# Kernel tuning notes

Hardware: AMD Instinct MI355X
Metric: run time of the kernel (lower is better)

The kernel has to match this reference:

```python
import jax, jax.numpy as jnp
import numpy as np

N = 100000        # nodes
E = 3200000       # edges per support (avg degree 32)
D_IN, D_OUT = 256, 128
ATT_H = 32
ALPHA, BETA = 0.5, 0.5  # FLAGS.alpha / FLAGS.beta


def setup_inputs() -> dict:
    key = jax.random.key(0)
    ks = jax.random.split(key, 10)
    x = jax.random.normal(ks[0], (N, D_IN), dtype=jnp.float32)
    glorot = lambda k, shp: jax.random.uniform(k, shp, jnp.float32,
                                               -np.sqrt(6.0 / sum(shp)), np.sqrt(6.0 / sum(shp)))
    Wa = glorot(ks[1], (D_IN, D_OUT))
    Wb = glorot(ks[2], (D_IN, D_OUT))
    Wc = glorot(ks[3], (D_IN, D_OUT))
    attn_w1 = glorot(ks[4], (D_OUT, ATT_H))
    attn_b1 = jnp.zeros((ATT_H,), jnp.float32)
    attn_w2 = glorot(ks[5], (ATT_H, 1))
    rows = jax.random.randint(ks[6], (7, E), 0, N, dtype=jnp.int32)
    cols = jax.random.randint(ks[7], (7, E), 0, N, dtype=jnp.int32)
    # normalized-adjacency-like positive values, scaled ~1/degree
    vals = jax.random.uniform(ks[8], (7, E), jnp.float32) * (1.0 / 32.0)
    return {"x": x, "Wa": Wa, "Wb": Wb, "Wc": Wc,
            "attn_w1": attn_w1, "attn_b1": attn_b1, "attn_w2": attn_w2,
            "rows": rows, "cols": cols, "vals": vals}


def reference(x, Wa, Wb, Wc, attn_w1, attn_b1, attn_w2, rows, cols, vals):
    n = x.shape[0]

    def spmm(i, X):
        # support[i] @ X via COO gather-scale-scatter: memory-bound SpMM
        return jax.ops.segment_sum(vals[i][:, None] * X[cols[i]], rows[i], num_segments=n)

    def bilinear_pooling(i, X):
        s = spmm(i, X)
        return 0.5 * (s * s - spmm(i, X * X))

    pre_a = x @ Wa                    # [N, D_OUT]
    pre_b = x @ Wb
    _ = x @ Wc                        # computed in original, never used
    sec_ord = 0.5 * (pre_a * pre_a - pre_a * pre_b)
    pre_al = pre_a + sec_ord

    emb = jnp.stack([pre_a, pre_al], axis=1)          # [N, 2, D_OUT]
    h = jnp.tanh(emb @ attn_w1 + attn_b1)             # [N, 2, 32]
    att = jax.nn.softmax(h @ attn_w2, axis=1)         # [N, 2, 1]
    pre_sup = jnp.sum(att * emb, axis=1)              # [N, D_OUT]

    out_gcn = spmm(0, pre_sup)
    out_bi1 = spmm(5, bilinear_pooling(1, pre_sup) - bilinear_pooling(3, pre_sup))
    out_bi2 = spmm(6, bilinear_pooling(2, pre_sup) - bilinear_pooling(4, pre_sup))
    out_bi = (1.0 - BETA) * out_bi1 + BETA * out_bi2
    output = (1.0 - ALPHA) * out_gcn + ALPHA * out_bi
    return jax.nn.relu(output)
```

## Files before the change

### kernel.cpp

```cpp
#include <hip/hip_runtime.h>

typedef unsigned int uint;
typedef unsigned short ushort;

__device__ __forceinline__ float bfl(uint u){ return __uint_as_float(u << 16); }
__device__ __forceinline__ float bfh(uint u){ return __uint_as_float(u & 0xFFFF0000u); }
__device__ __forceinline__ uint f2bfbits(float f){
    uint b = __float_as_uint(f);
    return (b + 0x7FFFu + ((b >> 16) & 1u)) >> 16;
}
__device__ __forceinline__ uint packbf2(float a, float b){
    return f2bfbits(a) | (f2bfbits(b) << 16);
}
__device__ __forceinline__ int smap(int4 m, int s){
    return (s == 0) ? m.x : (s == 1) ? m.y : (s == 2) ? m.z : m.w;
}
__device__ __forceinline__ int2 ldnt(const int2* p){
    long long v = __builtin_nontemporal_load((const long long*)p);
    int2 r; r.x = (int)(v & 0xFFFFFFFFll); r.y = (int)(v >> 32); return r;
}

#define CH 6144
#define SBSHIFT 7
#define SBROWS 128
#define HISTP 784
#define SBUF_CAP 5120
#define CACHE_PT 20
#define PGRID 2048


#define BM 64
#define BK 32
__global__ __launch_bounds__(256) void gemm_kernel(const float* __restrict__ x,
                                                   const float* __restrict__ Wa,
                                                   const float* __restrict__ Wb,
                                                   float* __restrict__ AB, int N) {
    __shared__ float xsT[BK][BM + 4];
    __shared__ float wsm[BK][256];
    int t = threadIdx.x;
    int rowbase = blockIdx.x * BM;
    int tx = t & 15, ty = t >> 4;
    float acc[4][16];
    #pragma unroll
    for (int i = 0; i < 4; i++)
        #pragma unroll
        for (int j = 0; j < 16; j++) acc[i][j] = 0.f;

    for (int k0 = 0; k0 < 256; k0 += BK) {
        {
            int r = t & 63;
            int koff = (t >> 6) * 8;
            int gr = rowbase + r; if (gr >= N) gr = N - 1;
            const float* src = x + (size_t)gr * 256 + k0 + koff;
            float4 u0 = *(const float4*)(src);
            float4 u1 = *(const float4*)(src + 4);
            xsT[koff + 0][r] = u0.x; xsT[koff + 1][r] = u0.y;
            xsT[koff + 2][r] = u0.z; xsT[koff + 3][r] = u0.w;
            xsT[koff + 4][r] = u1.x; xsT[koff + 5][r] = u1.y;
            xsT[koff + 6][r] = u1.z; xsT[koff + 7][r] = u1.w;
        }
        {
            #pragma unroll
            for (int i = 0; i < 8; i++) {
                int f = t + i * 256;
                int rr = f >> 6, c4 = f & 63;
                const float* src = (c4 < 32) ? &Wa[(size_t)(k0 + rr) * 128 + c4 * 4]
                                             : &Wb[(size_t)(k0 + rr) * 128 + (c4 - 32) * 4];
                *(float4*)&wsm[rr][c4 * 4] = *(const float4*)src;
            }
        }
        __syncthreads();
        #pragma unroll
        for (int kk = 0; kk < BK; ++kk) {
            float4 a = *(const float4*)&xsT[kk][ty * 4];
            float av[4] = {a.x, a.y, a.z, a.w};
            float bv[16];
            #pragma unroll
            for (int q = 0; q < 4; q++)
                *(float4*)&bv[q * 4] = *(const float4*)&wsm[kk][q * 64 + tx * 4];
            #pragma unroll
            for (int i = 0; i < 4; i++)
                #pragma unroll
                for (int j = 0; j < 16; j++)
                    acc[i][j] = fmaf(av[i], bv[j], acc[i][j]);
        }
        __syncthreads();
    }
    #pragma unroll
    for (int i = 0; i < 4; i++) {
        int gr = rowbase + ty * 4 + i;
        if (gr < N) {
            #pragma unroll
            for (int q = 0; q < 4; q++) {
                float4 o = {acc[i][q*4], acc[i][q*4+1], acc[i][q*4+2], acc[i][q*4+3]};
                *(float4*)&AB[(size_t)gr * 256 + q * 64 + tx * 4] = o;
            }
        }
    }
}

__global__ __launch_bounds__(256) void attn_kernel(const float* __restrict__ AB,
        const float* __restrict__ w1, const float* __restrict__ b1,
        const float* __restrict__ w2, uint* __restrict__ Pb, int N) {
    __shared__ float w1s[128 * 32];
    __shared__ float b1s[32], w2s[32];
    __shared__ float aS[4][128], alS[4][128];
    int t = threadIdx.x;
    #pragma unroll
    for (int i = 0; i < 16; i++) w1s[t + i * 256] = w1[t + i * 256];
    if (t < 32) { b1s[t] = b1[t]; w2s[t] = w2[t]; }

    int w = t >> 6, lane = t & 63;
    int node = blockIdx.x * 4 + w;
    bool active = node < N;
    int nclamp = active ? node : (N - 1);
    float2 a = *(const float2*)(AB + (size_t)nclamp * 256 + lane * 2);
    float2 b = *(const float2*)(AB + (size_t)nclamp * 256 + 128 + lane * 2);
    float2 al;
    al.x = a.x + 0.5f * (a.x * a.x - a.x * b.x);
    al.y = a.y + 0.5f * (a.y * a.y - a.y * b.y);
    aS[w][lane * 2] = a.x;   aS[w][lane * 2 + 1] = a.y;
    alS[w][lane * 2] = al.x; alS[w][lane * 2 + 1] = al.y;
    __syncthreads();

    int j = lane & 31;
    const float* src = (lane < 32) ? aS[w] : alS[w];
    float acc = b1s[j];
    #pragma unroll 8
    for (int d = 0; d < 128; ++d) acc = fmaf(src[d], w1s[d * 32 + j], acc);
    float h = tanhf(acc);
    float prod = h * w2s[j];
    #pragma unroll
    for (int off = 1; off < 32; off <<= 1) prod += __shfl_xor(prod, off);
    float eo = __shfl_xor(prod, 32);
    float e0 = (lane < 32) ? prod : eo;
    float e1 = (lane < 32) ? eo : prod;
    float m = fmaxf(e0, e1);
    float p0 = expf(e0 - m), p1 = expf(e1 - m);
    float inv = 1.0f / (p0 + p1);
    float at0 = p0 * inv, at1 = p1 * inv;
    if (active) {
        float px = at0 * a.x + at1 * al.x;
        float py = at0 * a.y + at1 * al.y;
        Pb[(size_t)node * 64 + lane] = packbf2(px, py);
    }
}


__device__ __forceinline__ void block_scan1024(int* a, int t, int* wsum) {
    int lane = t & 63, wid = t >> 6;
    int c0 = a[t * 4], c1 = a[t * 4 + 1], c2 = a[t * 4 + 2], c3 = a[t * 4 + 3];
    int tsum = c0 + c1 + c2 + c3, incl = tsum;
    #pragma unroll
    for (int off = 1; off < 64; off <<= 1) {
        int y = __shfl_up(incl, off);
        if (lane >= off) incl += y;
    }
    if (lane == 63) wsum[wid] = incl;
    __syncthreads();
    int wb = 0;
    #pragma unroll
    for (int w = 0; w < 4; w++) if (w < wid) wb += wsum[w];
    int excl = wb + incl - tsum;
    a[t * 4] = excl; a[t * 4 + 1] = excl + c0;
    a[t * 4 + 2] = excl + c0 + c1; a[t * 4 + 3] = excl + c0 + c1 + c2;
    __syncthreads();
}

__global__ __launch_bounds__(256) void count_chunk(const int* __restrict__ rows, int4 map,
        int* __restrict__ lenTab, int* __restrict__ gtot, int NSB, int nchunks, int E) {
    __shared__ int hist[HISTP];
    int c = blockIdx.x, s = blockIdx.y, t = threadIdx.x;
    size_t sb = (size_t)smap(map, s) * E;
    int e0 = c * CH, e1 = e0 + CH; if (e1 > E) e1 = E;
    for (int i = t; i < HISTP; i += 256) hist[i] = 0;
    __syncthreads();
    for (int e = e0 + t; e < e1; e += 256)
        atomicAdd(&hist[(uint)rows[sb + e] >> SBSHIFT], 1);
    __syncthreads();
    for (int b = t; b < NSB; b += 256) {
        int l = hist[b];
        lenTab[((size_t)s * NSB + b) * nchunks + c] = l;
        if (l) atomicAdd(&gtot[s * NSB + b], l);
    }
}

__global__ __launch_bounds__(256) void bucket_scanex(const int* __restrict__ gtot,
        int* __restrict__ bbase, int NSB) {
    __shared__ int a[1024];
    __shared__ int wsum[4];
    int s = blockIdx.x, t = threadIdx.x;
    #pragma unroll
    for (int k = 0; k < 4; k++) {
        int i = t + k * 256;
        a[i] = (i < NSB) ? gtot[s * NSB + i] : 0;
    }
    __syncthreads();
    block_scan1024(a, t, wsum);
    #pragma unroll
    for (int k = 0; k < 4; k++) {
        int i = t + k * 256;
        if (i <= NSB) bbase[s * (NSB + 1) + i] = a[i];
    }
}

__global__ __launch_bounds__(64) void pos_scan(const int* __restrict__ lenTab,
        const int* __restrict__ bbase, int* __restrict__ segPos, int NSB, int nchunks) {
    int b = blockIdx.x, s = blockIdx.y, lane = threadIdx.x;
    const int* lt = lenTab + ((size_t)s * NSB + b) * nchunks;
    int* sp = segPos + ((size_t)s * NSB + b) * nchunks;
    int run = bbase[s * (NSB + 1) + b];
    for (int c0 = 0; c0 < nchunks; c0 += 64) {
        int c = c0 + lane;
        int v = (c < nchunks) ? lt[c] : 0;
        int incl = v;
        #pragma unroll
        for (int off = 1; off < 64; off <<= 1) {
            int y = __shfl_up(incl, off);
            if (lane >= off) incl += y;
        }
        if (c < nchunks) sp[c] = run + incl - v;
        run += __shfl(incl, 63);
    }
}

__global__ __launch_bounds__(256) void place_chunk(const int* __restrict__ rows,
        const int* __restrict__ cols, const float* __restrict__ vals, int4 map,
        const int* __restrict__ segPos, int2* __restrict__ stage2,
        int NSB, int nchunks, int E) {
    __shared__ int2 sbuf[CH];
    __shared__ ushort bmap[CH];
    __shared__ int cur[1024];
    __shared__ int off[1024];
    __shared__ int spos[HISTP];
    __shared__ int wsum[4];
    int c = blockIdx.x, s = blockIdx.y, t = threadIdx.x;
    size_t sb = (size_t)smap(map, s) * E;
    int e0 = c * CH, e1 = e0 + CH; if (e1 > E) e1 = E;
    int csz = e1 - e0;
    #pragma unroll
    for (int k = 0; k < 4; k++) cur[t + k * 256] = 0;
    __syncthreads();
    for (int e = e0 + t; e < e1; e += 256)
        atomicAdd(&cur[(uint)rows[sb + e] >> SBSHIFT], 1);
    __syncthreads();
    block_scan1024(cur, t, wsum);
    #pragma unroll
    for (int k = 0; k < 4; k++) { int i = t + k * 256; off[i] = cur[i]; }
    for (int b = t; b < NSB; b += 256)
        spos[b] = segPos[((size_t)s * NSB + b) * nchunks + c];
    __syncthreads();
    for (int e = e0 + t; e < e1; e += 256) {
        int r = rows[sb + e];
        int b = (uint)r >> SBSHIFT;
        int pos = atomicAdd(&cur[b], 1);
        uint cw = (uint)cols[sb + e] | ((uint)(r & (SBROWS - 1)) << 20);
        sbuf[pos] = make_int2((int)cw, __float_as_int(vals[sb + e]));
        bmap[pos] = (ushort)b;
    }
    __syncthreads();
    int2* dst = stage2 + (size_t)s * E;
    for (int i = t; i < csz; i += 256) {
        int b = bmap[i];
        dst[spos[b] + (i - off[b])] = sbuf[i];
    }
}

__global__ __launch_bounds__(256) void fill_bucket(const int2* __restrict__ stage2,
        const int* __restrict__ bbase, int* __restrict__ rp, int2* __restrict__ pk,
        int NSB, int N, int E) {
    __shared__ int2 sbuf[SBUF_CAP];
    __shared__ int cur[128];
    __shared__ int loc[132];
    __shared__ int wsum2[2];
    int b = blockIdx.x, s = blockIdx.y, t = threadIdx.x;
    int lane = t & 63, wid = t >> 6;
    int rowbase = b << SBSHIFT;
    int nrows = N - rowbase; if (nrows > SBROWS) nrows = SBROWS;
    size_t sb = (size_t)s * E;
    int beg = bbase[s * (NSB + 1) + b];
    int end = bbase[s * (NSB + 1) + b + 1];
    int tot = end - beg;
    if (t < 128) cur[t] = 0;
    __syncthreads();
    int2 myE[CACHE_PT];
    #pragma unroll
    for (int k = 0; k < CACHE_PT; k++) {
        int idx = t + k * 256;
        if (idx < tot) {
            int2 u = stage2[sb + beg + idx];
            myE[k] = u;
            atomicAdd(&cur[((uint)u.x) >> 20], 1);
        }
    }
    for (int idx = t + CACHE_PT * 256; idx < tot; idx += 256) {
        int2 u = stage2[sb + beg + idx];
        atomicAdd(&cur[((uint)u.x) >> 20], 1);
    }
    __syncthreads();
    int v = 0, incl = 0;
    if (t < 128) {
        v = cur[t]; incl = v;
        #pragma unroll
        for (int off = 1; off < 64; off <<= 1) {
            int y = __shfl_up(incl, off);
            if (lane >= off) incl += y;
        }
        if (lane == 63) wsum2[wid] = incl;
    }
    __syncthreads();
    if (t < 128) {
        int excl = incl - v + ((wid == 1) ? wsum2[0] : 0);
        loc[t] = excl; cur[t] = excl;
        if (t < nrows) rp[(size_t)s * (N + 1) + rowbase + t] = beg + excl;
    }
    if (t == 0) loc[128] = tot;
    if (b == 0 && t == 0) rp[(size_t)s * (N + 1) + N] = E;
    __syncthreads();
    #pragma unroll
    for (int k = 0; k < CACHE_PT; k++) {
        int idx = t + k * 256;
        if (idx < tot) {
            int2 u = myE[k];
            int lr = ((uint)u.x) >> 20;
            int pos = atomicAdd(&cur[lr], 1);
            int2 w = make_int2(u.x & 0xFFFFF, u.y);
            if (pos < SBUF_CAP) sbuf[pos] = w; else pk[sb + beg + pos] = w;
        }
    }
    for (int idx = t + CACHE_PT * 256; idx < tot; idx += 256) {
        int2 u = stage2[sb + beg + idx];
        int lr = ((uint)u.x) >> 20;
        int pos = atomicAdd(&cur[lr], 1);
        int2 w = make_int2(u.x & 0xFFFFF, u.y);
        if (pos < SBUF_CAP) sbuf[pos] = w; else pk[sb + beg + pos] = w;
    }
    __syncthreads();
    for (int r = wid; r < nrows; r += 4) {
        int rb = loc[r], re = loc[r + 1];
        int deg = re - rb;
        if (deg < 2 || deg > 64 || re > SBUF_CAP) continue;
        int key = 0x7FFFFFFF, val = 0;
        if (lane < deg) { int2 u = sbuf[rb + lane]; key = u.x; val = u.y; }
        #pragma unroll
        for (int k = 2; k <= 64; k <<= 1) {
            #pragma unroll
            for (int j = k >> 1; j > 0; j >>= 1) {
                int okey = __shfl_xor(key, j);
                int oval = __shfl_xor(val, j);
                bool up = ((lane & k) == 0);
                bool lower = ((lane & j) == 0);
                bool keepmin = (lower == up);
                bool take = keepmin ? (okey < key) : (okey > key);
                if (take) { key = okey; val = oval; }
            }
        }
        if (lane < deg) sbuf[rb + lane] = make_int2(key, val);
    }
    __syncthreads();
    int lim = (tot < SBUF_CAP) ? tot : SBUF_CAP;
    for (int i = t; i < lim; i += 256)
        __builtin_nontemporal_store(*(const long long*)&sbuf[i], (long long*)&pk[sb + beg + i]);
}


__device__ __forceinline__ void row_gather_sum(const int2* __restrict__ pk,
        int e, int end, const uint* __restrict__ Xb, int lane,
        float& ax, float& ay) {
    for (; e + 4 <= end; e += 4) {
        int2 c0 = ldnt(&pk[e]);     int2 c1 = ldnt(&pk[e + 1]);
        int2 c2 = ldnt(&pk[e + 2]); int2 c3 = ldnt(&pk[e + 3]);
        uint u0 = Xb[(c0.x << 6) + lane]; uint u1 = Xb[(c1.x << 6) + lane];
        uint u2 = Xb[(c2.x << 6) + lane]; uint u3 = Xb[(c3.x << 6) + lane];
        float v0 = __int_as_float(c0.y), v1 = __int_as_float(c1.y);
        float v2 = __int_as_float(c2.y), v3 = __int_as_float(c3.y);
        ax = fmaf(v0, bfl(u0), ax); ay = fmaf(v0, bfh(u0), ay);
        ax = fmaf(v1, bfl(u1), ax); ay = fmaf(v1, bfh(u1), ay);
        ax = fmaf(v2, bfl(u2), ax); ay = fmaf(v2, bfh(u2), ay);
        ax = fmaf(v3, bfl(u3), ax); ay = fmaf(v3, bfh(u3), ay);
    }
    for (; e < end; ++e) {
        int2 c0 = ldnt(&pk[e]);
        uint u0 = Xb[(c0.x << 6) + lane];
        float v0 = __int_as_float(c0.y);
        ax = fmaf(v0, bfl(u0), ax); ay = fmaf(v0, bfh(u0), ay);
    }
}

__device__ __forceinline__ void row_gather_bp(const int2* __restrict__ pk,
        int e, int end, const uint* __restrict__ Xb, int lane,
        float& sx, float& sy, float& qx, float& qy) {
    for (; e + 4 <= end; e += 4) {
        int2 c0 = ldnt(&pk[e]);     int2 c1 = ldnt(&pk[e + 1]);
        int2 c2 = ldnt(&pk[e + 2]); int2 c3 = ldnt(&pk[e + 3]);
        uint u0 = Xb[(c0.x << 6) + lane]; uint u1 = Xb[(c1.x << 6) + lane];
        uint u2 = Xb[(c2.x << 6) + lane]; uint u3 = Xb[(c3.x << 6) + lane];
        float v0 = __int_as_float(c0.y), v1 = __int_as_float(c1.y);
        float v2 = __int_as_float(c2.y), v3 = __int_as_float(c3.y);
        float x0 = bfl(u0), y0 = bfh(u0), x1 = bfl(u1), y1 = bfh(u1);
        float x2 = bfl(u2), y2 = bfh(u2), x3 = bfl(u3), y3 = bfh(u3);
        sx = fmaf(v0, x0, sx); sy = fmaf(v0, y0, sy);
        qx = fmaf(v0 * x0, x0, qx); qy = fmaf(v0 * y0, y0, qy);
        sx = fmaf(v1, x1, sx); sy = fmaf(v1, y1, sy);
        qx = fmaf(v1 * x1, x1, qx); qy = fmaf(v1 * y1, y1, qy);
        sx = fmaf(v2, x2, sx); sy = fmaf(v2, y2, sy);
        qx = fmaf(v2 * x2, x2, qx); qy = fmaf(v2 * y2, y2, qy);
        sx = fmaf(v3, x3, sx); sy = fmaf(v3, y3, sy);
        qx = fmaf(v3 * x3, x3, qx); qy = fmaf(v3 * y3, y3, qy);
    }
    for (; e < end; ++e) {
        int2 c0 = ldnt(&pk[e]);
        uint u0 = Xb[(c0.x << 6) + lane];
        float v0 = __int_as_float(c0.y);
        float x0 = bfl(u0), y0 = bfh(u0);
        sx = fmaf(v0, x0, sx); sy = fmaf(v0, y0, sy);
        qx = fmaf(v0 * x0, x0, qx); qy = fmaf(v0 * y0, y0, qy);
    }
}

__global__ __launch_bounds__(256) void spmm_bp2(const int* __restrict__ rpA,
        const int2* __restrict__ pkA, const int* __restrict__ rpB,
        const int2* __restrict__ pkB, const uint* __restrict__ Xb,
        uint* __restrict__ outb, int N) {
    int w = threadIdx.x >> 6, lane = threadIdx.x & 63;
    int stride = gridDim.x * 4;
    for (int row = blockIdx.x * 4 + w; row < N; row += stride) {
        float sax = 0.f, say = 0.f, qax = 0.f, qay = 0.f;
        float sbx = 0.f, sby = 0.f, qbx = 0.f, qby = 0.f;
        row_gather_bp(pkA, rpA[row], rpA[row + 1], Xb, lane, sax, say, qax, qay);
        row_gather_bp(pkB, rpB[row], rpB[row + 1], Xb, lane, sbx, sby, qbx, qby);
        float tx = 0.5f * ((sax * sax - qax) - (sbx * sbx - qbx));
        float ty = 0.5f * ((say * say - qay) - (sby * sby - qby));
        outb[((size_t)row << 6) + lane] = packbf2(tx, ty);
    }
}

__global__ __launch_bounds__(256) void spmm_out(const int* __restrict__ rp0,
        const int2* __restrict__ pk0, const int* __restrict__ rp5,
        const int2* __restrict__ pk5, const int* __restrict__ rp6,
        const int2* __restrict__ pk6, const uint* __restrict__ Pb,
        const uint* __restrict__ t1b, const uint* __restrict__ t2b,
        float* __restrict__ out, int N) {
    int w = threadIdx.x >> 6, lane = threadIdx.x & 63;
    int stride = gridDim.x * 4;
    for (int row = blockIdx.x * 4 + w; row < N; row += stride) {
        float a0x = 0.f, a0y = 0.f, a5x = 0.f, a5y = 0.f, a6x = 0.f, a6y = 0.f;
        row_gather_sum(pk0, rp0[row], rp0[row + 1], Pb,  lane, a0x, a0y);
        row_gather_sum(pk5, rp5[row], rp5[row + 1], t1b, lane, a5x, a5y);
        row_gather_sum(pk6, rp6[row], rp6[row + 1], t2b, lane, a6x, a6y);
        float rx = fmaxf(0.5f * a0x + 0.25f * a5x + 0.25f * a6x, 0.f);
        float ry = fmaxf(0.5f * a0y + 0.25f * a5y + 0.25f * a6y, 0.f);
        *(float2*)(out + ((size_t)row << 7) + (lane << 1)) = make_float2(rx, ry);
    }
}


extern "C" void kernel_launch(void* const* d_in, const int* in_sizes, int n_in,
                              void* d_out, int out_size, void* d_ws, size_t ws_size,
                              hipStream_t stream) {
    (void)n_in; (void)out_size; (void)ws_size;
    const float* x   = (const float*)d_in[0];
    const float* Wa  = (const float*)d_in[1];
    const float* Wb  = (const float*)d_in[2];
    const float* w1  = (const float*)d_in[4];
    const float* b1  = (const float*)d_in[5];
    const float* w2  = (const float*)d_in[6];
    const int* rows  = (const int*)d_in[7];
    const int* cols  = (const int*)d_in[8];
    const float* vals = (const float*)d_in[9];
    float* out = (float*)d_out;

    const int N = in_sizes[0] / 256;
    const int E = in_sizes[7] / 7;
    const int NSB = (N + SBROWS - 1) >> SBSHIFT;
    const int nchunks = (E + CH - 1) / CH;

    uint* Pb  = (uint*)d_ws;
    uint* t1b = Pb + (size_t)N * 64;
    uint* t2b = t1b + (size_t)N * 64;
    int2* pk  = (int2*)(t2b + (size_t)N * 64);
    size_t regionFloats = (size_t)N * 256;
    if ((size_t)8 * E > regionFloats) regionFloats = (size_t)8 * E;
    int2* stage2 = pk + (size_t)4 * E;
    float* AB    = (float*)stage2;
    int* rp      = (int*)((float*)stage2 + regionFloats);
    int* lenTab  = rp + 4 * (size_t)(N + 1);
    int* segPos  = lenTab + (size_t)4 * NSB * nchunks;
    int* gtot    = segPos + (size_t)4 * NSB * nchunks;
    int* bbase   = gtot + (size_t)4 * NSB;

    dim3 b256(256);
    int sgrid = (N + 3) / 4;
    int pgrid = PGRID; if (pgrid > sgrid) pgrid = sgrid;

    gemm_kernel<<<(N + BM - 1) / BM, b256, 0, stream>>>(x, Wa, Wb, AB, N);
    attn_kernel<<<sgrid, b256, 0, stream>>>(AB, w1, b1, w2, Pb, N);

    auto build = [&](int4 map, int nsup) {
        hipMemsetAsync(gtot, 0, (size_t)nsup * NSB * sizeof(int), stream);
        count_chunk<<<dim3(nchunks, nsup), b256, 0, stream>>>(rows, map, lenTab, gtot,
                                                              NSB, nchunks, E);
        bucket_scanex<<<nsup, b256, 0, stream>>>(gtot, bbase, NSB);
        pos_scan<<<dim3(NSB, nsup), dim3(64), 0, stream>>>(lenTab, bbase, segPos, NSB, nchunks);
        place_chunk<<<dim3(nchunks, nsup), b256, 0, stream>>>(rows, cols, vals, map,
                                                              segPos, stage2, NSB, nchunks, E);
        fill_bucket<<<dim3(NSB, nsup), b256, 0, stream>>>(stage2, bbase, rp, pk, NSB, N, E);
    };

    const int NP1 = N + 1;

    build(make_int4(1, 3, 2, 4), 4);
    spmm_bp2<<<pgrid, b256, 0, stream>>>(rp + 0 * NP1, pk + 0 * (size_t)E,
                                         rp + 1 * NP1, pk + 1 * (size_t)E, Pb, t1b, N);
    spmm_bp2<<<pgrid, b256, 0, stream>>>(rp + 2 * NP1, pk + 2 * (size_t)E,
                                         rp + 3 * NP1, pk + 3 * (size_t)E, Pb, t2b, N);

    build(make_int4(0, 5, 6, 6), 3);
    spmm_out<<<pgrid, b256, 0, stream>>>(rp + 0 * NP1, pk + 0 * (size_t)E,
                                         rp + 1 * NP1, pk + 1 * (size_t)E,
                                         rp + 2 * NP1, pk + 2 * (size_t)E,
                                         Pb, t1b, t2b, out, N);
}
```

Baseline: 2.195 ms.

## Batch CSR build of all seven supports and drop global bucket atomics

When the workspace is large enough, the bucketed CSR build runs for all seven supports in a single batched set of kernels instead of two passes of four and three. Global bucket totals now come from a separate reduction over the per-chunk length table, replacing the memset and per-bucket atomics. Chunk block indices are also swizzled across XCDs. The batching uses more workspace and falls back to the old two-pass path otherwise.

```diff
diff --git a/kernel.cpp b/kernel.cpp
--- a/kernel.cpp
+++ b/kernel.cpp
@@ -12,12 +12,19 @@
 __device__ __forceinline__ uint packbf2(float a, float b){
     return f2bfbits(a) | (f2bfbits(b) << 16);
 }
-__device__ __forceinline__ int smap(int4 m, int s){
-    return (s == 0) ? m.x : (s == 1) ? m.y : (s == 2) ? m.z : m.w;
+__device__ __forceinline__ int smap8(int4 lo, int4 hi, int s){
+    int4 m = (s < 4) ? lo : hi;
+    int k = s & 3;
+    return (k == 0) ? m.x : (k == 1) ? m.y : (k == 2) ? m.z : m.w;
 }
 __device__ __forceinline__ int2 ldnt(const int2* p){
     long long v = __builtin_nontemporal_load((const long long*)p);
     int2 r; r.x = (int)(v & 0xFFFFFFFFll); r.y = (int)(v >> 32); return r;
+}
+__device__ __forceinline__ int xcd_swz(int bid, int n){
+    int q = n >> 3, r = n & 7;
+    int x = bid & 7, i = bid >> 3;
+    return (x < r) ? (x * (q + 1) + i) : (r * (q + 1) + (x - r) * q + i);
 }
 
 #define CH 6144
@@ -167,25 +174,35 @@
     __syncthreads();
 }
 
-__global__ __launch_bounds__(256) void count_chunk(const int* __restrict__ rows, int4 map,
-        int* __restrict__ lenTab, int* __restrict__ gtot, int NSB, int nchunks, int E) {
+__global__ __launch_bounds__(256) void count_chunk(const int* __restrict__ rows,
+        int4 mlo, int4 mhi, int* __restrict__ lenTab, int NSB, int nchunks, int E) {
     __shared__ int hist[HISTP];
-    int c = blockIdx.x, s = blockIdx.y, t = threadIdx.x;
-    size_t sb = (size_t)smap(map, s) * E;
+    int c = xcd_swz(blockIdx.x, nchunks), s = blockIdx.y, t = threadIdx.x;
+    size_t sb = (size_t)smap8(mlo, mhi, s) * E;
     int e0 = c * CH, e1 = e0 + CH; if (e1 > E) e1 = E;
     for (int i = t; i < HISTP; i += 256) hist[i] = 0;
     __syncthreads();
     for (int e = e0 + t; e < e1; e += 256)
         atomicAdd(&hist[(uint)rows[sb + e] >> SBSHIFT], 1);
     __syncthreads();
-    for (int b = t; b < NSB; b += 256) {
-        int l = hist[b];
-        lenTab[((size_t)s * NSB + b) * nchunks + c] = l;
-        if (l) atomicAdd(&gtot[s * NSB + b], l);
-    }
-}
-
-__global__ __launch_bounds__(256) void bucket_scanex(const int* __restrict__ gtot,
+    for (int b = t; b < NSB; b += 256)
+        lenTab[((size_t)s * NSB + b) * nchunks + c] = hist[b];
+}
+
+__global__ __launch_bounds__(256) void btot_kernel(const int* __restrict__ lenTab,
+        int* __restrict__ btot, int NSB, int nchunks) {
+    int s = blockIdx.y;
+    int b = blockIdx.x * 256 + threadIdx.x;
+    if (b >= NSB) return;
+    const int* lt = lenTab + ((size_t)s * NSB + b) * nchunks;
+    int a0 = 0, a1 = 0, a2 = 0, a3 = 0;
+    int c = 0;
+    for (; c + 4 <= nchunks; c += 4) { a0 += lt[c]; a1 += lt[c+1]; a2 += lt[c+2]; a3 += lt[c+3]; }
+    for (; c < nchunks; ++c) a0 += lt[c];
+    btot[s * NSB + b] = a0 + a1 + a2 + a3;
+}
+
+__global__ __launch_bounds__(256) void bucket_scanex(const int* __restrict__ btot,
         int* __restrict__ bbase, int NSB) {
     __shared__ int a[1024];
     __shared__ int wsum[4];
@@ -193,7 +210,7 @@
     #pragma unroll
     for (int k = 0; k < 4; k++) {
         int i = t + k * 256;
-        a[i] = (i < NSB) ? gtot[s * NSB + i] : 0;
+        a[i] = (i < NSB) ? btot[s * NSB + i] : 0;
     }
     __syncthreads();
     block_scan1024(a, t, wsum);
@@ -225,8 +242,8 @@
 }
 
 __global__ __launch_bounds__(256) void place_chunk(const int* __restrict__ rows,
-        const int* __restrict__ cols, const float* __restrict__ vals, int4 map,
-        const int* __restrict__ segPos, int2* __restrict__ stage2,
+        const int* __restrict__ cols, const float* __restrict__ vals,
+        int4 mlo, int4 mhi, const int* __restrict__ segPos, int2* __restrict__ stage2,
         int NSB, int nchunks, int E) {
     __shared__ int2 sbuf[CH];
     __shared__ ushort bmap[CH];
@@ -234,8 +251,8 @@
     __shared__ int off[1024];
     __shared__ int spos[HISTP];
     __shared__ int wsum[4];
-    int c = blockIdx.x, s = blockIdx.y, t = threadIdx.x;
-    size_t sb = (size_t)smap(map, s) * E;
+    int c = xcd_swz(blockIdx.x, nchunks), s = blockIdx.y, t = threadIdx.x;
+    size_t sb = (size_t)smap8(mlo, mhi, s) * E;
     int e0 = c * CH, e1 = e0 + CH; if (e1 > E) e1 = E;
     int csz = e1 - e0;
     #pragma unroll
@@ -458,7 +475,7 @@
 extern "C" void kernel_launch(void* const* d_in, const int* in_sizes, int n_in,
                               void* d_out, int out_size, void* d_ws, size_t ws_size,
                               hipStream_t stream) {
-    (void)n_in; (void)out_size; (void)ws_size;
+    (void)n_in; (void)out_size;
     const float* x   = (const float*)d_in[0];
     const float* Wa  = (const float*)d_in[1];
     const float* Wb  = (const float*)d_in[2];
@@ -475,49 +492,75 @@
     const int NSB = (N + SBROWS - 1) >> SBSHIFT;
     const int nchunks = (E + CH - 1) / CH;
 
+    auto layoutBytes = [&](int ns) -> size_t {
+        size_t bts = 3 * (size_t)N * 64 * 4;
+        bts += (size_t)ns * E * 8;
+        size_t region = (size_t)N * 1024;
+        if ((size_t)ns * E * 8 > region) region = (size_t)ns * E * 8;
+        bts += region;
+        bts += (size_t)ns * (N + 1) * 4;
+        bts += 2 * (size_t)ns * NSB * (size_t)nchunks * 4;
+        bts += (size_t)ns * NSB * 4;
+        bts += (size_t)ns * (NSB + 1) * 4;
+        return bts + 4096;
+    };
+    const int NSUP = (ws_size >= layoutBytes(7)) ? 7 : 4;
+
     uint* Pb  = (uint*)d_ws;
     uint* t1b = Pb + (size_t)N * 64;
     uint* t2b = t1b + (size_t)N * 64;
     int2* pk  = (int2*)(t2b + (size_t)N * 64);
     size_t regionFloats = (size_t)N * 256;
-    if ((size_t)8 * E > regionFloats) regionFloats = (size_t)8 * E;
-    int2* stage2 = pk + (size_t)4 * E;
+    if ((size_t)NSUP * E * 2 > regionFloats) regionFloats = (size_t)NSUP * E * 2;
+    int2* stage2 = pk + (size_t)NSUP * E;
     float* AB    = (float*)stage2;
     int* rp      = (int*)((float*)stage2 + regionFloats);
-    int* lenTab  = rp + 4 * (size_t)(N + 1);
-    int* segPos  = lenTab + (size_t)4 * NSB * nchunks;
-    int* gtot    = segPos + (size_t)4 * NSB * nchunks;
-    int* bbase   = gtot + (size_t)4 * NSB;
+    int* lenTab  = rp + (size_t)NSUP * (N + 1);
+    int* segPos  = lenTab + (size_t)NSUP * NSB * nchunks;
+    int* btot    = segPos + (size_t)NSUP * NSB * nchunks;
+    int* bbase   = btot + (size_t)NSUP * NSB;
 
     dim3 b256(256);
     int sgrid = (N + 3) / 4;
     int pgrid = PGRID; if (pgrid > sgrid) pgrid = sgrid;
+    int bgrid = (NSB + 255) / 256;
 
     gemm_kernel<<<(N + BM - 1) / BM, b256, 0, stream>>>(x, Wa, Wb, AB, N);
     attn_kernel<<<sgrid, b256, 0, stream>>>(AB, w1, b1, w2, Pb, N);
 
-    auto build = [&](int4 map, int nsup) {
-        hipMemsetAsync(gtot, 0, (size_t)nsup * NSB * sizeof(int), stream);
-        count_chunk<<<dim3(nchunks, nsup), b256, 0, stream>>>(rows, map, lenTab, gtot,
+    auto build = [&](int4 mlo, int4 mhi, int nsup) {
+        count_chunk<<<dim3(nchunks, nsup), b256, 0, stream>>>(rows, mlo, mhi, lenTab,
                                                               NSB, nchunks, E);
-        bucket_scanex<<<nsup, b256, 0, stream>>>(gtot, bbase, NSB);
+        btot_kernel<<<dim3(bgrid, nsup), b256, 0, stream>>>(lenTab, btot, NSB, nchunks);
+        bucket_scanex<<<nsup, b256, 0, stream>>>(btot, bbase, NSB);
         pos_scan<<<dim3(NSB, nsup), dim3(64), 0, stream>>>(lenTab, bbase, segPos, NSB, nchunks);
-        place_chunk<<<dim3(nchunks, nsup), b256, 0, stream>>>(rows, cols, vals, map,
+        place_chunk<<<dim3(nchunks, nsup), b256, 0, stream>>>(rows, cols, vals, mlo, mhi,
                                                               segPos, stage2, NSB, nchunks, E);
         fill_bucket<<<dim3(NSB, nsup), b256, 0, stream>>>(stage2, bbase, rp, pk, NSB, N, E);
     };
 
-    const int NP1 = N + 1;
-
-    build(make_int4(1, 3, 2, 4), 4);
-    spmm_bp2<<<pgrid, b256, 0, stream>>>(rp + 0 * NP1, pk + 0 * (size_t)E,
-                                         rp + 1 * NP1, pk + 1 * (size_t)E, Pb, t1b, N);
-    spmm_bp2<<<pgrid, b256, 0, stream>>>(rp + 2 * NP1, pk + 2 * (size_t)E,
-                                         rp + 3 * NP1, pk + 3 * (size_t)E, Pb, t2b, N);
-
-    build(make_int4(0, 5, 6, 6), 3);
-    spmm_out<<<pgrid, b256, 0, stream>>>(rp + 0 * NP1, pk + 0 * (size_t)E,
-                                         rp + 1 * NP1, pk + 1 * (size_t)E,
-                                         rp + 2 * NP1, pk + 2 * (size_t)E,
-                                         Pb, t1b, t2b, out, N);
-}
+    const size_t NP1 = (size_t)(N + 1);
+
+    if (NSUP == 7) {
+        build(make_int4(1, 3, 2, 4), make_int4(0, 5, 6, 6), 7);
+        spmm_bp2<<<pgrid, b256, 0, stream>>>(rp + 0 * NP1, pk + 0 * (size_t)E,
+                                             rp + 1 * NP1, pk + 1 * (size_t)E, Pb, t1b, N);
+        spmm_bp2<<<pgrid, b256, 0, stream>>>(rp + 2 * NP1, pk + 2 * (size_t)E,
+                                             rp + 3 * NP1, pk + 3 * (size_t)E, Pb, t2b, N);
+        spmm_out<<<pgrid, b256, 0, stream>>>(rp + 4 * NP1, pk + 4 * (size_t)E,
+                                             rp + 5 * NP1, pk + 5 * (size_t)E,
+                                             rp + 6 * NP1, pk + 6 * (size_t)E,
+                                             Pb, t1b, t2b, out, N);
+    } else {
+        build(make_int4(1, 3, 2, 4), make_int4(0, 0, 0, 0), 4);
+        spmm_bp2<<<pgrid, b256, 0, stream>>>(rp + 0 * NP1, pk + 0 * (size_t)E,
+                                             rp + 1 * NP1, pk + 1 * (size_t)E, Pb, t1b, N);
+        spmm_bp2<<<pgrid, b256, 0, stream>>>(rp + 2 * NP1, pk + 2 * (size_t)E,
+                                             rp + 3 * NP1, pk + 3 * (size_t)E, Pb, t2b, N);
+        build(make_int4(0, 5, 6, 6), make_int4(0, 0, 0, 0), 3);
+        spmm_out<<<pgrid, b256, 0, stream>>>(rp + 0 * NP1, pk + 0 * (size_t)E,
+                                             rp + 1 * NP1, pk + 1 * (size_t)E,
+                                             rp + 2 * NP1, pk + 2 * (size_t)E,
+                                             Pb, t1b, t2b, out, N);
+    }
+}
```

New measurement: 2.161 ms. Within noise of the previous version (-1.6%).
